# Kernel tuning notes

Measured on AMD Instinct MI355X. Metric: run time of the kernel, lower is better.

Reference implementation:

```python
import jax, jax.numpy as jnp
import numpy as np

NUM_QUERIES = 150
NEG = 1e9


def setup_inputs() -> dict:
    key = jax.random.key(0)
    ks = jax.random.split(key, 5)
    B, C, H, W = 4, 256, 64, 64
    img_feat = jax.random.normal(ks[0], (B, C, H, W), dtype=jnp.float32)
    exe_feat = jax.random.normal(ks[1], (B, C), dtype=jnp.float32)
    mask = jax.random.bernoulli(ks[2], 0.9, (B, H, W)).astype(jnp.float32)
    # similarity initialized as identity (plus tiny noise so it's non-degenerate)
    similarity = jnp.eye(C, dtype=jnp.float32) + 0.01 * jax.random.normal(ks[3], (C, C), dtype=jnp.float32)
    # nn.Linear weight, shape (out, in)
    v_w = jax.random.normal(ks[4], (C, C), dtype=jnp.float32) / np.sqrt(C)
    return {"img_feat": img_feat, "exe_feat": exe_feat, "mask": mask,
            "similarity": similarity, "v_w": v_w}


def _get_queries(attn, B, H, W):
    # peak detection on similarity-to-exemplar channel (last column), no grad
    simil = jax.lax.stop_gradient(attn[:, :, -1]).reshape(B, H, W)
    c = simil[:, 1:-1, 1:-1]
    is_max = ((c > simil[:, :-2, 1:-1]) &   # strictly greater than above
              (c >= simil[:, 2:, 1:-1]) &   # >= below
              (c > simil[:, 1:-1, :-2]) &   # strictly greater than left
              (c >= simil[:, 1:-1, 2:]))    # >= right
    pen = jnp.zeros_like(simil).at[:, 1:-1, 1:-1].set(
        jnp.where(is_max, 0.0, NEG))
    scores = (simil - pen).reshape(B, H * W)
    _, q_ids = jax.lax.top_k(scores, NUM_QUERIES)  # [B, Q]
    return q_ids


def reference(img_feat, exe_feat, mask, similarity, v_w):
    B, C, H, W = img_feat.shape
    HW = H * W
    unrolled = img_feat.reshape(B, C, HW)                      # [B,C,HW]
    exe = (exe_feat * 1.2)[:, :, None]                         # [B,C,1]
    concat = jnp.concatenate([unrolled, exe], axis=2)          # [B,C,HW+1]
    # values = Linear(concat^T): x @ W^T
    values = jnp.einsum('bcn,dc->bnd', concat, v_w)            # [B,HW+1,C]
    # attn = unrolled^T @ similarity @ concat
    attn = jnp.einsum('bcn,cd,bdm->bnm', unrolled, similarity, concat)  # [B,HW,HW+1]

    q_ids = _get_queries(attn, B, H, W)                        # [B,Q] int
    queries = jnp.take_along_axis(values[:, :-1], q_ids[:, :, None], axis=1)  # [B,Q,C]

    # masked softmax: outer product of pixel mask, exemplar column always kept
    m = jax.lax.stop_gradient(mask).reshape(B, HW)
    mm = m[:, :, None] * m[:, None, :]                         # [B,HW,HW]
    mm = jnp.concatenate([mm, jnp.ones((B, HW, 1), mm.dtype)], axis=2)
    attn = attn - (mm != 1).astype(attn.dtype) * NEG
    attn = jax.nn.softmax(attn, axis=2)

    new_img = jnp.einsum('bnm,bmd->bnd', attn, values)         # [B,HW,C]
    new_img = new_img.transpose(0, 2, 1).reshape(B, C, H, W)
    return new_img + img_feat, queries
```

## Files before the change

kernel.cpp:

```cpp
#include <hip/hip_runtime.h>

#define CC   256
#define HWS  4096
#define MPAD 4160
#define NB   4
#define NTIL 65

typedef __attribute__((ext_vector_type(8))) short   short8;
typedef __attribute__((ext_vector_type(4))) float   floatx4;

static __device__ __forceinline__ short8 ld8(const unsigned short* p) {
  return *(const short8*)p;
}
static __device__ __forceinline__ void st8(unsigned short* p, short8 v) {
  *(short8*)p = v;
}
static __device__ __forceinline__ unsigned short f2b(float x) {
  union { float f; unsigned u; } v; v.f = x;
  unsigned r = v.u + 0x7FFFu + ((v.u >> 16) & 1u);
  return (unsigned short)(r >> 16);
}
static __device__ __forceinline__ float b2f(unsigned short x) {
  union { unsigned u; float f; } v; v.u = ((unsigned)x) << 16;
  return v.f;
}

__global__ void prep_colb(const float* __restrict__ sim, const float* __restrict__ vw,
                          const float* __restrict__ mask,
                          unsigned short* __restrict__ St, unsigned short* __restrict__ Vw,
                          float* __restrict__ colb) {
  int blk = blockIdx.x, tid = threadIdx.x;
  if (blk < CC) {
    int dd = blk, c = tid;
    St[dd*CC + c] = f2b(sim[c*CC + dd]);
    Vw[dd*CC + c] = f2b(vw[dd*CC + c]);
    return;
  }
  int b = blk - CC;
  for (int m = tid; m < MPAD; m += 256) {
    float v;
    if (m < HWS)      v = (mask[b*HWS + m] - 1.0f) * 1e9f;
    else if (m == HWS) v = 0.0f;
    else               v = -3.0e38f;
    colb[b*MPAD + m] = v;
  }
}

__global__ void build_kt(const float* __restrict__ img, const float* __restrict__ exe,
                         unsigned short* __restrict__ Kt, unsigned short* __restrict__ Kf) {
  int b = blockIdx.x, mt = blockIdx.y, dt = blockIdx.z;
  int tid = threadIdx.x;
  int m0 = mt*64, d0 = dt*64;
  int w = tid >> 6, lane = tid & 63, lo = lane & 15, hi = lane >> 4;
  unsigned short* kft = Kf + (size_t)(b*NTIL + mt)*16384;
  if (mt == 64) {
    for (int i = 0; i < 16; ++i) {
      int m = m0 + (tid>>6) + i*4;
      int d = d0 + (tid&63);
      unsigned short v = 0;
      if (m == 4096) v = f2b(1.2f * exe[b*CC + d]);
      Kt[((size_t)b*MPAD + m)*CC + d] = v;
    }
#pragma unroll
    for (int ss = 0; ss < 2; ++ss) {
      int s = dt*8 + w*2 + ss;
      int k = s >> 2, t = s & 3;
      unsigned short tmp[8] = {0,0,0,0,0,0,0,0};
      if (t == 0 && lo == 0) {
#pragma unroll
        for (int j = 0; j < 8; ++j)
          tmp[j] = f2b(1.2f * exe[b*CC + k*32 + hi*8 + j]);
      }
      st8(kft + s*512 + lane*8, *(short8*)tmp);
    }
    return;
  }
  __shared__ float tile[64][65];
  for (int i = 0; i < 16; ++i) {
    int dl = (tid>>6) + i*4, ml = tid&63;
    tile[dl][ml] = img[((size_t)b*CC + d0+dl)*HWS + m0+ml];
  }
  __syncthreads();
  for (int i = 0; i < 16; ++i) {
    int ml = (tid>>6) + i*4, dl = tid&63;
    Kt[((size_t)b*MPAD + m0+ml)*CC + d0+dl] = f2b(tile[dl][ml]);
  }
#pragma unroll
  for (int ss = 0; ss < 2; ++ss) {
    int s = dt*8 + w*2 + ss;
    int k = s >> 2, t = s & 3;
    int ml = t*16 + lo;
    int dlb = (k - dt*2)*32 + hi*8;
    unsigned short tmp[8];
#pragma unroll
    for (int j = 0; j < 8; ++j) tmp[j] = f2b(tile[dlb + j][ml]);
    st8(kft + s*512 + lane*8, *(short8*)tmp);
  }
}

__global__ __launch_bounds__(256) void gemm_small(const unsigned short* __restrict__ Kf,
    const unsigned short* __restrict__ Bm, unsigned short* __restrict__ Tout,
    unsigned short* __restrict__ Vf, int mode) {
  int b  = blockIdx.x;
  int by = blockIdx.y;
  int w  = threadIdx.x >> 6;
  int c0 = blockIdx.z*64;
  int lane = threadIdx.x & 63;
  int lo = lane & 15, hi = lane >> 4;
  __shared__ unsigned short lsh[64][72];
  floatx4 acc[4] = {};
  const unsigned short* kft = Kf + (size_t)(b*NTIL + by)*16384 + lane*8;
#pragma unroll
  for (int k = 0; k < 8; ++k) {
    short8 af = ld8(kft + (k*4 + w)*512);
#pragma unroll
    for (int t = 0; t < 4; ++t) {
      short8 bf = ld8(Bm + (size_t)(c0 + t*16 + lo)*CC + k*32 + hi*8);
      acc[t] = __builtin_amdgcn_mfma_f32_16x16x32_bf16(af, bf, acc[t], 0, 0, 0);
    }
  }
  if (mode == 0) {
#pragma unroll
    for (int t = 0; t < 4; ++t)
#pragma unroll
      for (int r = 0; r < 4; ++r)
        lsh[w*16 + hi*4 + r][t*16 + lo] = f2b(acc[t][r]);
    __syncthreads();
    int tid = threadIdx.x;
    int nl = tid >> 2, seg = tid & 3;
    unsigned short* dst = Tout + ((size_t)b*HWS + by*64 + nl)*CC + c0 + seg*16;
    st8(dst,     ld8(&lsh[nl][seg*16]));
    st8(dst + 8, ld8(&lsh[nl][seg*16 + 8]));
  } else {
#pragma unroll
    for (int t = 0; t < 4; ++t)
#pragma unroll
      for (int r = 0; r < 4; ++r)
        lsh[t*16 + lo][w*16 + hi*4 + r] = f2b(acc[t][r]);
    __syncthreads();
    unsigned short* vfb2 = Vf + (size_t)(b*NTIL + by)*16384;
#pragma unroll
    for (int ss = 0; ss < 2; ++ss) {
      int idx = w*2 + ss;
      int h = idx >> 2, t4 = idx & 3;
      int s = h*16 + (c0 >> 4) + t4;
      short8 v = ld8(&lsh[t4*16 + (lane & 15)][h*32 + (lane >> 4)*8]);
      st8(vfb2 + s*512 + lane*8, v);
    }
  }
}

__global__ __launch_bounds__(256) void scores_kernel(const float* __restrict__ img,
    const float* __restrict__ sim, const float* __restrict__ exe,
    float* __restrict__ score32) {
  int b = blockIdx.x, n0 = blockIdx.y*32;
  int d = threadIdx.x;
  __shared__ float U[32][257];
  __shared__ float R[32][257];
  __shared__ float E[256];
  for (int idx = threadIdx.x; idx < 32*256; idx += 256) {
    int nl = idx & 31, c = idx >> 5;
    U[nl][c] = img[((size_t)b*CC + c)*HWS + n0 + nl];
  }
  E[d] = 1.2f * exe[b*CC + d];
  __syncthreads();
  float acc[32];
#pragma unroll
  for (int nl = 0; nl < 32; ++nl) acc[nl] = 0.f;
  for (int c = 0; c < CC; ++c) {
    float s_cd = sim[c*CC + d];
#pragma unroll
    for (int nl = 0; nl < 32; ++nl) acc[nl] = fmaf(U[nl][c], s_cd, acc[nl]);
  }
#pragma unroll
  for (int nl = 0; nl < 32; ++nl) R[nl][d] = acc[nl];
  __syncthreads();
  if (d < 32) {
    float s = 0.f;
    for (int dd = 0; dd < CC; ++dd) s = fmaf(R[d][dd], E[dd], s);
    score32[b*HWS + n0 + d] = s;
  }
}

__global__ __launch_bounds__(64) void select_kernel(const float* __restrict__ scores,
                                                    int* __restrict__ qids) {
  int b = blockIdx.x, lane = threadIdx.x;
  __shared__ float sc[HWS];
  __shared__ unsigned long long kx[HWS];
  __shared__ unsigned long long list[256];
  __shared__ unsigned int hist[256];
  __shared__ unsigned int st[4];
  __shared__ unsigned long long sh_base;

  const floatx4* s4 = (const floatx4*)(scores + (size_t)b*HWS);
  floatx4* c4 = (floatx4*)sc;
#pragma unroll
  for (int i = 0; i < 16; ++i) c4[i*64 + lane] = s4[i*64 + lane];
  __syncthreads();

  for (int i = 0; i < 64; ++i) {
    int idx = i*64 + lane;
    int y = i, x = lane;
    float c0 = sc[idx];
    float v = c0;
    if (y >= 1 && y <= 62 && x >= 1 && x <= 62) {
      bool ismax = (c0 > sc[idx-64]) && (c0 >= sc[idx+64]) &&
                   (c0 > sc[idx-1])  && (c0 >= sc[idx+1]);
      if (!ismax) v = c0 - 1e9f;
    }
    unsigned u = __float_as_uint(v);
    u = (u & 0x80000000u) ? ~u : (u | 0x80000000u);
    kx[idx] = (((unsigned long long)u) << 12) | (unsigned long long)(4095 - idx);
  }
  __syncthreads();

  unsigned long long base = 0;
  unsigned int need = 150, C = 0;
  for (int s = 36; s >= 4; s -= 8) {
    for (int i = lane; i < 256; i += 64) hist[i] = 0;
    __syncthreads();
    unsigned long long pref = base >> (s + 8);
    for (int i = 0; i < 64; ++i) {
      unsigned long long k = kx[i*64 + lane];
      if ((k >> (s + 8)) == pref) atomicAdd(&hist[(unsigned)(k >> s) & 255u], 1u);
    }
    __syncthreads();
    if (lane == 0) {
      unsigned cum = 0; int B = 0;
      for (int bin = 255; bin >= 0; --bin) {
        cum += hist[bin];
        if (cum >= need) { B = bin; break; }
      }
      st[0] = (150u - need) + cum;
      st[1] = need - (cum - hist[B]);
      sh_base = base | ((unsigned long long)B << s);
    }
    __syncthreads();
    C = st[0]; need = st[1]; base = sh_base;
    if (C <= 256u) break;
  }

  if (lane == 0) st[2] = 0;
  __syncthreads();
  for (int i = 0; i < 64; ++i) {
    unsigned long long k = kx[i*64 + lane];
    if (k >= base) {
      unsigned p = atomicAdd(&st[2], 1u);
      list[p] = k;
    }
  }
  __syncthreads();
  for (int i = lane; i < 256; i += 64) if (i >= (int)C) list[i] = 0ull;
  __syncthreads();

  for (int kk = 2; kk <= 256; kk <<= 1) {
    for (int j = kk >> 1; j > 0; j >>= 1) {
#pragma unroll
      for (int tt = 0; tt < 2; ++tt) {
        int t = lane + tt*64;
        int i2 = ((t & ~(j - 1)) << 1) | (t & (j - 1));
        int p2 = i2 | j;
        bool desc = ((i2 & kk) == 0);
        unsigned long long a = list[i2], c = list[p2];
        bool sw = desc ? (a < c) : (a > c);
        if (sw) { list[i2] = c; list[p2] = a; }
      }
      __syncthreads();
    }
  }

  for (int q = lane; q < 150; q += 64)
    qids[b*150 + q] = 4095 - (int)(list[q] & 0xFFFull);
}

__global__ __launch_bounds__(256, 1) void flash_kernel(
    const unsigned short* __restrict__ Tb, const unsigned short* __restrict__ Kt,
    const unsigned short* __restrict__ Kf, const unsigned short* __restrict__ Vf,
    const float* __restrict__ mask, const float* __restrict__ colb,
    float* __restrict__ acc0, float* __restrict__ accH, float* __restrict__ lsums) {
  int blk = blockIdx.x;
  int b    = (blk & 7) >> 1;
  int half = blk & 1;
  int g    = blk >> 3;
  int tid = threadIdx.x;
  int wave = tid >> 6, lane = tid & 63;
  int lo = lane & 15, hi = lane >> 4;
  int n0 = g*128 + wave*32;
  int t0 = half ? 33 : 0, t1 = half ? NTIL : 33;

  __shared__ unsigned short pbuf[4][1152];
  unsigned short* plw = &pbuf[wave][0];

  short8 q0[8], q1[8];
  const unsigned short* tb0 = Tb + ((size_t)b*HWS + n0 + lo)*CC + hi*8;
#pragma unroll
  for (int k = 0; k < 8; ++k) { q0[k] = ld8(tb0 + k*32); q1[k] = ld8(tb0 + 16*CC + k*32); }

  const unsigned short* kfb = Kf + (size_t)b*NTIL*16384 + lane*8;
  const unsigned short* vfb = Vf + (size_t)b*NTIL*16384 + lane*8;

  short8 X[16], Y[16];
#pragma unroll
  for (int i = 0; i < 16; ++i) X[i] = ld8(kfb + (size_t)t0*16384 + i*512);
#pragma unroll
  for (int i = 0; i < 16; ++i) Y[i] = ld8(kfb + (size_t)t0*16384 + (16 + i)*512);

  const float* mk = mask + b*HWS;

  float crb0[4], Msub0[4], crb1[4], Msub1[4];
  {
    const unsigned short* kep = Kt + ((size_t)b*MPAD + HWS)*CC + hi*8;
    float ddot = 0.f, edot = 0.f;
    const unsigned short* kdp = Kt + ((size_t)b*MPAD + n0 + lo)*CC + hi*8;
#pragma unroll
    for (int k = 0; k < 8; ++k) {
      short8 kd = ld8(kdp + k*32);
      short8 ke = ld8(kep + k*32);
#pragma unroll
      for (int j = 0; j < 8; ++j) {
        float qf = b2f((unsigned short)q0[k][j]);
        ddot = fmaf(qf, b2f((unsigned short)kd[j]), ddot);
        edot = fmaf(qf, b2f((unsigned short)ke[j]), edot);
      }
    }
    ddot += __shfl_xor(ddot, 16); ddot += __shfl_xor(ddot, 32);
    edot += __shfl_xor(edot, 16); edot += __shfl_xor(edot, 32);
    float Mrow = ((mk[n0 + lo] == 1.0f) ? ddot : edot) + 2.0f;
    float* fM = (float*)plw;
    fM[lo] = Mrow;
#pragma unroll
    for (int r = 0; r < 4; ++r) {
      Msub0[r] = fM[hi*4 + r];
      crb0[r]  = (mk[n0 + hi*4 + r] - 1.0f)*1e9f - Msub0[r];
    }
    ddot = 0.f; edot = 0.f;
    const unsigned short* kdp1 = Kt + ((size_t)b*MPAD + n0 + 16 + lo)*CC + hi*8;
#pragma unroll
    for (int k = 0; k < 8; ++k) {
      short8 kd = ld8(kdp1 + k*32);
      short8 ke = ld8(kep + k*32);
#pragma unroll
      for (int j = 0; j < 8; ++j) {
        float qf = b2f((unsigned short)q1[k][j]);
        ddot = fmaf(qf, b2f((unsigned short)kd[j]), ddot);
        edot = fmaf(qf, b2f((unsigned short)ke[j]), edot);
      }
    }
    ddot += __shfl_xor(ddot, 16); ddot += __shfl_xor(ddot, 32);
    edot += __shfl_xor(edot, 16); edot += __shfl_xor(edot, 32);
    float Mrow1 = ((mk[n0 + 16 + lo] == 1.0f) ? ddot : edot) + 2.0f;
    fM[lo] = Mrow1;
#pragma unroll
    for (int r = 0; r < 4; ++r) {
      Msub1[r] = fM[hi*4 + r];
      crb1[r]  = (mk[n0 + 16 + hi*4 + r] - 1.0f)*1e9f - Msub1[r];
    }
  }

  float lsum0[4] = {0.f, 0.f, 0.f, 0.f};
  float lsum1[4] = {0.f, 0.f, 0.f, 0.f};
  floatx4 o0[16] = {};
  floatx4 o1[16] = {};
  const float* cbb = colb + b*MPAD;

  for (int mt = t0; mt < t1; ++mt) {
    int m0 = mt*64;
    const unsigned short* vs = vfb + (size_t)mt*16384;
    floatx4 s0[4] = {}, s1[4] = {};
#pragma unroll
    for (int k = 0; k < 4; ++k)
#pragma unroll
      for (int t = 0; t < 4; ++t) {
        s0[t] = __builtin_amdgcn_mfma_f32_16x16x32_bf16(q0[k], X[k*4 + t], s0[t], 0, 0, 0);
        s1[t] = __builtin_amdgcn_mfma_f32_16x16x32_bf16(q1[k], X[k*4 + t], s1[t], 0, 0, 0);
      }
#pragma unroll
    for (int i = 0; i < 16; ++i) X[i] = ld8(vs + i*512);
#pragma unroll
    for (int k = 4; k < 8; ++k)
#pragma unroll
      for (int t = 0; t < 4; ++t) {
        s0[t] = __builtin_amdgcn_mfma_f32_16x16x32_bf16(q0[k], Y[(k-4)*4 + t], s0[t], 0, 0, 0);
        s1[t] = __builtin_amdgcn_mfma_f32_16x16x32_bf16(q1[k], Y[(k-4)*4 + t], s1[t], 0, 0, 0);
      }
#pragma unroll
    for (int i = 0; i < 16; ++i) Y[i] = ld8(vs + (16 + i)*512);
    float cb[4];
#pragma unroll
    for (int t = 0; t < 4; ++t) cb[t] = cbb[m0 + t*16 + lo];
    short8 pf00, pf01, pf10, pf11;
    {
      float pr[4][4];
#pragma unroll
      for (int t = 0; t < 4; ++t)
#pragma unroll
        for (int r = 0; r < 4; ++r)
          pr[t][r] = s0[t][r] + cb[t] + crb0[r];
      if (mt == NTIL-1 && lo == 0) {
#pragma unroll
        for (int r = 0; r < 4; ++r) pr[0][r] = s0[0][r] - Msub0[r];
      }
#pragma unroll
      for (int t = 0; t < 4; ++t)
#pragma unroll
        for (int r = 0; r < 4; ++r) {
          float p = __expf(pr[t][r]);
          lsum0[r] += p;
          plw[(hi*4 + r)*72 + t*16 + lo] = f2b(p);
        }
      pf00 = *(const short8*)&plw[lo*72 + hi*8];
      pf01 = *(const short8*)&plw[lo*72 + 32 + hi*8];
    }
    {
      float pr[4][4];
#pragma unroll
      for (int t = 0; t < 4; ++t)
#pragma unroll
        for (int r = 0; r < 4; ++r)
          pr[t][r] = s1[t][r] + cb[t] + crb1[r];
      if (mt == NTIL-1 && lo == 0) {
#pragma unroll
        for (int r = 0; r < 4; ++r) pr[0][r] = s1[0][r] - Msub1[r];
      }
#pragma unroll
      for (int t = 0; t < 4; ++t)
#pragma unroll
        for (int r = 0; r < 4; ++r) {
          float p = __expf(pr[t][r]);
          lsum1[r] += p;
          plw[(hi*4 + r)*72 + t*16 + lo] = f2b(p);
        }
      pf10 = *(const short8*)&plw[lo*72 + hi*8];
      pf11 = *(const short8*)&plw[lo*72 + 32 + hi*8];
    }
#pragma unroll
    for (int sl = 0; sl < 16; ++sl) {
      o0[sl] = __builtin_amdgcn_mfma_f32_16x16x32_bf16(pf00, X[sl], o0[sl], 0, 0, 0);
      o1[sl] = __builtin_amdgcn_mfma_f32_16x16x32_bf16(pf10, X[sl], o1[sl], 0, 0, 0);
    }
    if (mt + 1 < t1) {
      const unsigned short* ks = kfb + (size_t)(mt+1)*16384;
#pragma unroll
      for (int i = 0; i < 16; ++i) X[i] = ld8(ks + i*512);
    }
#pragma unroll
    for (int sl = 0; sl < 16; ++sl) {
      o0[sl] = __builtin_amdgcn_mfma_f32_16x16x32_bf16(pf01, Y[sl], o0[sl], 0, 0, 0);
      o1[sl] = __builtin_amdgcn_mfma_f32_16x16x32_bf16(pf11, Y[sl], o1[sl], 0, 0, 0);
    }
    if (mt + 1 < t1) {
      const unsigned short* ks = kfb + (size_t)(mt+1)*16384;
#pragma unroll
      for (int i = 0; i < 16; ++i) Y[i] = ld8(ks + (16 + i)*512);
    }
  }
#pragma unroll
  for (int r = 0; r < 4; ++r) {
#pragma unroll
    for (int off = 1; off < 16; off <<= 1) {
      lsum0[r] += __shfl_xor(lsum0[r], off);
      lsum1[r] += __shfl_xor(lsum1[r], off);
    }
  }
  float* op = (half ? accH : acc0) + (size_t)b*CC*HWS;
#pragma unroll
  for (int t = 0; t < 16; ++t)
#pragma unroll
    for (int r = 0; r < 4; ++r) {
      op[(size_t)(t*16 + lo)*HWS + n0 + hi*4 + r]      = o0[t][r];
      op[(size_t)(t*16 + lo)*HWS + n0 + 16 + hi*4 + r] = o1[t][r];
    }
  if (lo == 0) {
    float* lp = lsums + ((size_t)(half*NB + b))*HWS;
#pragma unroll
    for (int r = 0; r < 4; ++r) {
      lp[n0 + hi*4 + r]      = lsum0[r];
      lp[n0 + 16 + hi*4 + r] = lsum1[r];
    }
  }
}

__global__ __launch_bounds__(256) void finalize_kernel(const float* __restrict__ accH,
    const float* __restrict__ lsums, const float* __restrict__ img,
    float* __restrict__ out0) {
  int b = blockIdx.x >> 8;
  int d = blockIdx.x & 255;
  size_t base = ((size_t)b*CC + d)*HWS;
  const float* l0 = lsums + (size_t)b*HWS;
  const float* l1 = lsums + (size_t)(NB + b)*HWS;
  for (int n = threadIdx.x; n < HWS; n += 256) {
    float inv = 1.0f / (l0[n] + l1[n]);
    float o = (out0[base + n] + accH[base + n]) * inv;
    out0[base + n] = b2f(f2b(o)) + img[base + n];
  }
}

__global__ __launch_bounds__(256) void gather_kernel(const float* __restrict__ img,
    const float* __restrict__ vw, const int* __restrict__ qids, float* __restrict__ out1) {
  int blk = blockIdx.x;
  int b = blk / 150, q = blk % 150;
  int dd = threadIdx.x;
  __shared__ float col[CC];
  int id = qids[b*150 + q];
  col[dd] = img[((size_t)b*CC + dd)*HWS + id];
  __syncthreads();
  const float* vr = vw + dd*CC;
  float acc = 0.f;
  for (int c = 0; c < CC; ++c) acc = fmaf(col[c], vr[c], acc);
  out1[((size_t)(b*150 + q))*CC + dd] = acc;
}

extern "C" void kernel_launch(void* const* d_in, const int* in_sizes, int n_in,
                              void* d_out, int out_size, void* d_ws, size_t ws_size,
                              hipStream_t stream) {
  const float* img  = (const float*)d_in[0];
  const float* exe  = (const float*)d_in[1];
  const float* mask = (const float*)d_in[2];
  const float* sim  = (const float*)d_in[3];
  const float* vw   = (const float*)d_in[4];
  float* out0 = (float*)d_out;
  float* out1 = out0 + (size_t)NB*CC*HWS;

  char* ws = (char*)d_ws;
  size_t o = 0;
  unsigned short* Kt  = (unsigned short*)(ws + o); o += (size_t)NB*MPAD*CC*2;
  unsigned short* Tb  = (unsigned short*)(ws + o); o += (size_t)NB*HWS*CC*2;
  unsigned short* Kf  = (unsigned short*)(ws + o); o += (size_t)NB*NTIL*16384*2;
  unsigned short* Vf  = (unsigned short*)(ws + o); o += (size_t)NB*NTIL*16384*2;
  unsigned short* St  = (unsigned short*)(ws + o); o += (size_t)CC*CC*2;
  unsigned short* Vw  = (unsigned short*)(ws + o); o += (size_t)CC*CC*2;
  float*          scores = (float*)(ws + o);       o += (size_t)NB*HWS*4;
  float*          colb   = (float*)(ws + o);       o += (size_t)NB*MPAD*4;
  int*            qids   = (int*)(ws + o);         o += (size_t)NB*150*4;
  float*          accH   = (float*)(ws + o);       o += (size_t)NB*CC*HWS*4;
  float*          lsums  = (float*)(ws + o);       o += (size_t)2*NB*HWS*4;

  prep_colb  <<<dim3(CC + NB),    dim3(256), 0, stream>>>(sim, vw, mask, St, Vw, colb);
  build_kt   <<<dim3(NB, 65, 4),  dim3(256), 0, stream>>>(img, exe, Kt, Kf);
  gemm_small <<<dim3(NB, 64, 4),  dim3(256), 0, stream>>>(Kf, St, Tb, nullptr, 0);
  gemm_small <<<dim3(NB, 65, 4),  dim3(256), 0, stream>>>(Kf, Vw, nullptr, Vf, 1);
  scores_kernel<<<dim3(NB, 128),  dim3(256), 0, stream>>>(img, sim, exe, scores);
  select_kernel<<<dim3(NB),       dim3(64),  0, stream>>>(scores, qids);
  flash_kernel <<<dim3(256),      dim3(256), 0, stream>>>(Tb, Kt, Kf, Vf, mask, colb,
                                                          out0, accH, lsums);
  finalize_kernel<<<dim3(NB*CC),  dim3(256), 0, stream>>>(accH, lsums, img, out0);
  gather_kernel<<<dim3(NB*150),   dim3(256), 0, stream>>>(img, vw, qids, out1);
}
```

Measured before the change: 370.7 us.

## Drop Kt buffer, read diagonal from Kf fragments, and merge small kernels

Removes the row-major bf16 Kt workspace entirely. The flash kernel's diagonal and exemplar dot products now read from the MFMA-fragment Kf layout, which avoids writing and re-reading several MB of K data. Prep work is folded into extra blocks of build_kt, the two gemm_small launches become one grid, and finalize and gather are combined into one kernel, cutting launch count from nine to six. The risk is indexing errors in the fragment-layout reads and slightly more branchy kernels.

```diff
diff --git a/kernel.cpp b/kernel.cpp
--- a/kernel.cpp
+++ b/kernel.cpp
@@ -25,42 +25,34 @@
   return v.f;
 }
 
-__global__ void prep_colb(const float* __restrict__ sim, const float* __restrict__ vw,
-                          const float* __restrict__ mask,
-                          unsigned short* __restrict__ St, unsigned short* __restrict__ Vw,
-                          float* __restrict__ colb) {
-  int blk = blockIdx.x, tid = threadIdx.x;
-  if (blk < CC) {
-    int dd = blk, c = tid;
-    St[dd*CC + c] = f2b(sim[c*CC + dd]);
-    Vw[dd*CC + c] = f2b(vw[dd*CC + c]);
-    return;
-  }
-  int b = blk - CC;
-  for (int m = tid; m < MPAD; m += 256) {
-    float v;
-    if (m < HWS)      v = (mask[b*HWS + m] - 1.0f) * 1e9f;
-    else if (m == HWS) v = 0.0f;
-    else               v = -3.0e38f;
-    colb[b*MPAD + m] = v;
-  }
-}
-
 __global__ void build_kt(const float* __restrict__ img, const float* __restrict__ exe,
-                         unsigned short* __restrict__ Kt, unsigned short* __restrict__ Kf) {
+                         const float* __restrict__ sim, const float* __restrict__ vw,
+                         const float* __restrict__ mask,
+                         unsigned short* __restrict__ Kf, unsigned short* __restrict__ St,
+                         unsigned short* __restrict__ Vw, float* __restrict__ colb) {
   int b = blockIdx.x, mt = blockIdx.y, dt = blockIdx.z;
   int tid = threadIdx.x;
+  if (b == NB) {
+    int pblk = mt*4 + dt;
+    if (pblk < CC) {
+      St[pblk*CC + tid] = f2b(sim[tid*CC + pblk]);
+      Vw[pblk*CC + tid] = f2b(vw[pblk*CC + tid]);
+      return;
+    }
+    int bb = pblk - CC;
+    for (int m = tid; m < MPAD; m += 256) {
+      float v;
+      if (m < HWS)      v = (mask[bb*HWS + m] - 1.0f) * 1e9f;
+      else if (m == HWS) v = 0.0f;
+      else               v = -3.0e38f;
+      colb[bb*MPAD + m] = v;
+    }
+    return;
+  }
   int m0 = mt*64, d0 = dt*64;
   int w = tid >> 6, lane = tid & 63, lo = lane & 15, hi = lane >> 4;
   unsigned short* kft = Kf + (size_t)(b*NTIL + mt)*16384;
   if (mt == 64) {
-    for (int i = 0; i < 16; ++i) {
-      int m = m0 + (tid>>6) + i*4;
-      int d = d0 + (tid&63);
-      unsigned short v = 0;
-      if (m == 4096) v = f2b(1.2f * exe[b*CC + d]);
-      Kt[((size_t)b*MPAD + m)*CC + d] = v;
-    }
 #pragma unroll
     for (int ss = 0; ss < 2; ++ss) {
       int s = dt*8 + w*2 + ss;
@@ -81,10 +73,6 @@
     tile[dl][ml] = img[((size_t)b*CC + d0+dl)*HWS + m0+ml];
   }
   __syncthreads();
-  for (int i = 0; i < 16; ++i) {
-    int ml = (tid>>6) + i*4, dl = tid&63;
-    Kt[((size_t)b*MPAD + m0+ml)*CC + d0+dl] = f2b(tile[dl][ml]);
-  }
 #pragma unroll
   for (int ss = 0; ss < 2; ++ss) {
     int s = dt*8 + w*2 + ss;
@@ -99,14 +87,17 @@
 }
 
 __global__ __launch_bounds__(256) void gemm_small(const unsigned short* __restrict__ Kf,
-    const unsigned short* __restrict__ Bm, unsigned short* __restrict__ Tout,
-    unsigned short* __restrict__ Vf, int mode) {
-  int b  = blockIdx.x;
-  int by = blockIdx.y;
-  int w  = threadIdx.x >> 6;
-  int c0 = blockIdx.z*64;
+    const unsigned short* __restrict__ St, const unsigned short* __restrict__ Vwm,
+    unsigned short* __restrict__ Tout, unsigned short* __restrict__ Vf) {
+  int b   = blockIdx.x;
+  int byr = blockIdx.y;
+  int mode = (byr >= 64);
+  int by  = mode ? byr - 64 : byr;
+  int w   = threadIdx.x >> 6;
+  int c0  = blockIdx.z*64;
   int lane = threadIdx.x & 63;
   int lo = lane & 15, hi = lane >> 4;
+  const unsigned short* Bm = mode ? Vwm : St;
   __shared__ unsigned short lsh[64][72];
   floatx4 acc[4] = {};
   const unsigned short* kft = Kf + (size_t)(b*NTIL + by)*16384 + lane*8;
@@ -119,7 +110,7 @@
       acc[t] = __builtin_amdgcn_mfma_f32_16x16x32_bf16(af, bf, acc[t], 0, 0, 0);
     }
   }
-  if (mode == 0) {
+  if (!mode) {
 #pragma unroll
     for (int t = 0; t < 4; ++t)
 #pragma unroll
@@ -274,9 +265,9 @@
 }
 
 __global__ __launch_bounds__(256, 1) void flash_kernel(
-    const unsigned short* __restrict__ Tb, const unsigned short* __restrict__ Kt,
-    const unsigned short* __restrict__ Kf, const unsigned short* __restrict__ Vf,
-    const float* __restrict__ mask, const float* __restrict__ colb,
+    const unsigned short* __restrict__ Tb, const unsigned short* __restrict__ Kf,
+    const unsigned short* __restrict__ Vf, const float* __restrict__ mask,
+    const float* __restrict__ colb,
     float* __restrict__ acc0, float* __restrict__ accH, float* __restrict__ lsums) {
   int blk = blockIdx.x;
   int b    = (blk & 7) >> 1;
@@ -309,13 +300,15 @@
 
   float crb0[4], Msub0[4], crb1[4], Msub1[4];
   {
-    const unsigned short* kep = Kt + ((size_t)b*MPAD + HWS)*CC + hi*8;
+    int nt  = n0 >> 6;
+    int t16 = (n0 & 63) >> 4;
+    const unsigned short* kfd = Kf + (size_t)(b*NTIL + nt)*16384 + lane*8;
+    const unsigned short* kfe = Kf + (size_t)(b*NTIL + 64)*16384 + hi*128;
     float ddot = 0.f, edot = 0.f;
-    const unsigned short* kdp = Kt + ((size_t)b*MPAD + n0 + lo)*CC + hi*8;
 #pragma unroll
     for (int k = 0; k < 8; ++k) {
-      short8 kd = ld8(kdp + k*32);
-      short8 ke = ld8(kep + k*32);
+      short8 kd = ld8(kfd + (k*4 + t16)*512);
+      short8 ke = ld8(kfe + (k*4)*512);
 #pragma unroll
       for (int j = 0; j < 8; ++j) {
         float qf = b2f((unsigned short)q0[k][j]);
@@ -334,11 +327,10 @@
       crb0[r]  = (mk[n0 + hi*4 + r] - 1.0f)*1e9f - Msub0[r];
     }
     ddot = 0.f; edot = 0.f;
-    const unsigned short* kdp1 = Kt + ((size_t)b*MPAD + n0 + 16 + lo)*CC + hi*8;
 #pragma unroll
     for (int k = 0; k < 8; ++k) {
-      short8 kd = ld8(kdp1 + k*32);
-      short8 ke = ld8(kep + k*32);
+      short8 kd = ld8(kfd + (k*4 + t16 + 1)*512);
+      short8 ke = ld8(kfe + (k*4)*512);
 #pragma unroll
       for (int j = 0; j < 8; ++j) {
         float qf = b2f((unsigned short)q1[k][j]);
@@ -480,25 +472,26 @@
   }
 }
 
-__global__ __launch_bounds__(256) void finalize_kernel(const float* __restrict__ accH,
+__global__ __launch_bounds__(256) void fin_gather(const float* __restrict__ accH,
     const float* __restrict__ lsums, const float* __restrict__ img,
-    float* __restrict__ out0) {
-  int b = blockIdx.x >> 8;
-  int d = blockIdx.x & 255;
-  size_t base = ((size_t)b*CC + d)*HWS;
-  const float* l0 = lsums + (size_t)b*HWS;
-  const float* l1 = lsums + (size_t)(NB + b)*HWS;
-  for (int n = threadIdx.x; n < HWS; n += 256) {
-    float inv = 1.0f / (l0[n] + l1[n]);
-    float o = (out0[base + n] + accH[base + n]) * inv;
-    out0[base + n] = b2f(f2b(o)) + img[base + n];
-  }
-}
-
-__global__ __launch_bounds__(256) void gather_kernel(const float* __restrict__ img,
-    const float* __restrict__ vw, const int* __restrict__ qids, float* __restrict__ out1) {
+    const float* __restrict__ vw, const int* __restrict__ qids,
+    float* __restrict__ out0, float* __restrict__ out1) {
   int blk = blockIdx.x;
-  int b = blk / 150, q = blk % 150;
+  if (blk < NB*CC) {
+    int b = blk >> 8;
+    int d = blk & 255;
+    size_t base = ((size_t)b*CC + d)*HWS;
+    const float* l0 = lsums + (size_t)b*HWS;
+    const float* l1 = lsums + (size_t)(NB + b)*HWS;
+    for (int n = threadIdx.x; n < HWS; n += 256) {
+      float inv = 1.0f / (l0[n] + l1[n]);
+      float o = (out0[base + n] + accH[base + n]) * inv;
+      out0[base + n] = b2f(f2b(o)) + img[base + n];
+    }
+    return;
+  }
+  int gb = blk - NB*CC;
+  int b = gb / 150, q = gb % 150;
   int dd = threadIdx.x;
   __shared__ float col[CC];
   int id = qids[b*150 + q];
@@ -523,7 +516,6 @@
 
   char* ws = (char*)d_ws;
   size_t o = 0;
-  unsigned short* Kt  = (unsigned short*)(ws + o); o += (size_t)NB*MPAD*CC*2;
   unsigned short* Tb  = (unsigned short*)(ws + o); o += (size_t)NB*HWS*CC*2;
   unsigned short* Kf  = (unsigned short*)(ws + o); o += (size_t)NB*NTIL*16384*2;
   unsigned short* Vf  = (unsigned short*)(ws + o); o += (size_t)NB*NTIL*16384*2;
@@ -535,14 +527,13 @@
   float*          accH   = (float*)(ws + o);       o += (size_t)NB*CC*HWS*4;
   float*          lsums  = (float*)(ws + o);       o += (size_t)2*NB*HWS*4;
 
-  prep_colb  <<<dim3(CC + NB),    dim3(256), 0, stream>>>(sim, vw, mask, St, Vw, colb);
-  build_kt   <<<dim3(NB, 65, 4),  dim3(256), 0, stream>>>(img, exe, Kt, Kf);
-  gemm_small <<<dim3(NB, 64, 4),  dim3(256), 0, stream>>>(Kf, St, Tb, nullptr, 0);
-  gemm_small <<<dim3(NB, 65, 4),  dim3(256), 0, stream>>>(Kf, Vw, nullptr, Vf, 1);
-  scores_kernel<<<dim3(NB, 128),  dim3(256), 0, stream>>>(img, sim, exe, scores);
-  select_kernel<<<dim3(NB),       dim3(64),  0, stream>>>(scores, qids);
-  flash_kernel <<<dim3(256),      dim3(256), 0, stream>>>(Tb, Kt, Kf, Vf, mask, colb,
-                                                          out0, accH, lsums);
-  finalize_kernel<<<dim3(NB*CC),  dim3(256), 0, stream>>>(accH, lsums, img, out0);
-  gather_kernel<<<dim3(NB*150),   dim3(256), 0, stream>>>(img, vw, qids, out1);
-}
+  build_kt   <<<dim3(NB+1, 65, 4), dim3(256), 0, stream>>>(img, exe, sim, vw, mask,
+                                                           Kf, St, Vw, colb);
+  gemm_small <<<dim3(NB, 129, 4),  dim3(256), 0, stream>>>(Kf, St, Vw, Tb, Vf);
+  scores_kernel<<<dim3(NB, 128),   dim3(256), 0, stream>>>(img, sim, exe, scores);
+  select_kernel<<<dim3(NB),        dim3(64),  0, stream>>>(scores, qids);
+  flash_kernel <<<dim3(256),       dim3(256), 0, stream>>>(Tb, Kf, Vf, mask, colb,
+                                                           out0, accH, lsums);
+  fin_gather   <<<dim3(NB*CC + NB*150), dim3(256), 0, stream>>>(accH, lsums, img, vw,
+                                                                qids, out0, out1);
+}
```

Result: faster. 357.0 us (-3.7%).
